# Performance work log

Hardware: AMD Instinct MI355X
Metric: run time of the kernel (lower is better)

## Reference

```python
import jax, jax.numpy as jnp
import numpy as np

L = 2        # num_layers
H = 512      # hidden_size
IN = 32      # input_size = output_size + 24
OUT = 8      # output_size
B = 512      # batch
S = 128      # encoder seq_len
F = 48       # future_len
TF = 24      # time-feature dim


def setup_inputs() -> dict:
    key = jax.random.key(0)
    ks = jax.random.split(key, 14)
    def rn(k, shape, s=0.05):
        return jax.random.normal(k, shape, dtype=jnp.float32) * s
    return {
        "x": rn(ks[0], (S, B, IN), 1.0),
        "future_time": rn(ks[1], (F - 1, B, TF), 1.0),
        "h0": rn(ks[2], (L, 1, H), 1.0),
        "c0": rn(ks[3], (L, 1, H), 1.0),
        # PyTorch nn.LSTM weights: gate order (i, f, g, o), rows of 4H
        "w_ih0": rn(ks[4], (4 * H, IN)),
        "w_hh0": rn(ks[5], (4 * H, H)),
        "b_ih0": rn(ks[6], (4 * H,)),
        "b_hh0": rn(ks[7], (4 * H,)),
        "w_ih1": rn(ks[8], (4 * H, H)),
        "w_hh1": rn(ks[9], (4 * H, H)),
        "b_ih1": rn(ks[10], (4 * H,)),
        "b_hh1": rn(ks[11], (4 * H,)),
        "fc_w": rn(ks[12], (OUT, H)),
        "fc_b": rn(ks[13], (OUT,)),
    }


def _cell(x, h, c, w_ih, w_hh, b):
    # PyTorch LSTMCell math, gate order i,f,g,o
    gates = x @ w_ih.T + h @ w_hh.T + b  # [B, 4H]
    i, f, g, o = jnp.split(gates, 4, axis=-1)
    c2 = jax.nn.sigmoid(f) * c + jax.nn.sigmoid(i) * jnp.tanh(g)
    h2 = jax.nn.sigmoid(o) * jnp.tanh(c2)
    return h2, c2


def reference(x, future_time, h0, c0,
              w_ih0, w_hh0, b_ih0, b_hh0,
              w_ih1, w_hh1, b_ih1, b_hh1,
              fc_w, fc_b):
    batch = x.shape[1]
    params = [(w_ih0, w_hh0, b_ih0 + b_hh0),
              (w_ih1, w_hh1, b_ih1 + b_hh1)]
    h_init = jnp.broadcast_to(h0, (L, batch, H))
    c_init = jnp.broadcast_to(c0, (L, batch, H))

    def multi_step(carry, x_t):
        hs, cs = carry
        new_h, new_c = [], []
        inp = x_t
        for l, (wi, wh, b) in enumerate(params):
            h2, c2 = _cell(inp, hs[l], cs[l], wi, wh, b)
            new_h.append(h2)
            new_c.append(c2)
            inp = h2
        return (jnp.stack(new_h), jnp.stack(new_c)), inp

    # encoder pass over the conditioning sequence
    (hs, cs), outs = jax.lax.scan(multi_step, (h_init, c_init), x)
    y0 = outs[-1] @ fc_w.T + fc_b  # [B, OUT], first prediction

    def dec_step(carry, t_feat):
        hs, cs, y = carry
        x_t = jnp.concatenate([y, t_feat], axis=-1)  # [B, OUT+TF] == [B, IN]
        (hs2, cs2), h_top = multi_step((hs, cs), x_t)
        y2 = h_top @ fc_w.T + fc_b
        return (hs2, cs2, y2), y2

    _, ys = jax.lax.scan(dec_step, (hs, cs, y0), future_time)
    return jnp.concatenate([y0[None], ys], axis=0)  # [future_len, B, OUT]
```

## Files before the change

kernel.cpp:

```cpp
#include <hip/hip_runtime.h>


typedef __attribute__((ext_vector_type(8))) short bf16x8;
typedef __attribute__((ext_vector_type(16))) float f32x16;

#define MFMA32(a, b, c) __builtin_amdgcn_mfma_f32_32x32x16_bf16((a), (b), (c), 0, 0, 0)
#define DEV static __device__ __forceinline__

constexpr int kSeq = 128;
constexpr int kT = 175;
constexpr int kRB = 65536;

constexpr size_t kWsHbuf = 0;
constexpr size_t kWsYacc = 2ull * 2 * 8 * kRB;
constexpr size_t kWsCnt  = kWsYacc + 2ull * 512 * 8 * 4;
constexpr size_t kWsRc   = kWsCnt + 2ull * 8 * 128;
constexpr size_t kWsEnd  = kWsRc + 2ull * 8 * 64;
constexpr size_t kWsZeroBegin = kWsYacc;
constexpr size_t kWsZeroSize  = kWsEnd - kWsYacc;

DEV unsigned short f2bf(float f) {
  unsigned u = __float_as_uint(f);
  u += 0x7fffu + ((u >> 16) & 1u);
  return (unsigned short)(u >> 16);
}
DEV float bf2f(unsigned short s) { return __uint_as_float(((unsigned)s) << 16); }
DEV float sigf(float v) { return 1.0f / (1.0f + __expf(-v)); }
DEV float tanhf_(float v) { float e = __expf(2.0f * v); return 1.0f - 2.0f / (e + 1.0f); }
DEV f32x16 zero16() {
  f32x16 z;
#pragma unroll
  for (int i = 0; i < 16; ++i) z[i] = 0.0f;
  return z;
}
DEV bf16x8 pack8(const float* p) {
  float4 a = *(const float4*)p;
  float4 b = *(const float4*)(p + 4);
  bf16x8 r;
  r[0] = (short)f2bf(a.x); r[1] = (short)f2bf(a.y);
  r[2] = (short)f2bf(a.z); r[3] = (short)f2bf(a.w);
  r[4] = (short)f2bf(b.x); r[5] = (short)f2bf(b.y);
  r[6] = (short)f2bf(b.z); r[7] = (short)f2bf(b.w);
  return r;
}

DEV unsigned ald(const unsigned* p) {
  return __hip_atomic_load(p, __ATOMIC_RELAXED, __HIP_MEMORY_SCOPE_AGENT);
}
DEV unsigned long long ald64(const unsigned long long* p) {
  return __hip_atomic_load(p, __ATOMIC_RELAXED, __HIP_MEMORY_SCOPE_AGENT);
}
DEV void ast64(unsigned long long* p, unsigned long long v) {
  __hip_atomic_store(p, v, __ATOMIC_RELAXED, __HIP_MEMORY_SCOPE_AGENT);
}
DEV float aldf(const float* p) {
  return __hip_atomic_load(p, __ATOMIC_RELAXED, __HIP_MEMORY_SCOPE_AGENT);
}
DEV void astf(float* p, float v) {
  __hip_atomic_store(p, v, __ATOMIC_RELAXED, __HIP_MEMORY_SCOPE_AGENT);
}
DEV void aadd(unsigned* p) {
  __hip_atomic_fetch_add(p, 1u, __ATOMIC_RELAXED, __HIP_MEMORY_SCOPE_AGENT);
}
DEV void relwait() {
  __atomic_signal_fence(__ATOMIC_SEQ_CST);
  __builtin_amdgcn_s_waitcnt(0);
  __atomic_signal_fence(__ATOMIC_SEQ_CST);
}
DEV bool pollc(const unsigned* c0, unsigned t0, const unsigned* c1, unsigned t1) {
  const int ln = (int)(threadIdx.x & 63);
  const unsigned* p = (ln == 1) ? c1 : c0;
  const unsigned thr = (ln == 0) ? t0 : ((ln == 1) ? t1 : 0u);
  for (int it = 0; it < (1 << 22); ++it) {
    const unsigned v = (ln < 2) ? ald(p) : 0xffffffffu;
    if (__ballot(v < thr) == 0ull) {
      __atomic_signal_fence(__ATOMIC_ACQUIRE);
      return true;
    }
    __builtin_amdgcn_s_sleep(2);
  }
  return false;
}

#define PARTS_WRITE(accv, ms_, ns_)                                           \
  { const int gate_ = (ns_)*2 + gbit;                                         \
    _Pragma("unroll") for (int rg = 0; rg < 16; ++rg) {                       \
      const int r_ = (ms_)*32 + (rg & 3) + 4 * hi5 + 8 * (rg >> 2);           \
      partsB[((kw * 4 + gate_) * 64 + r_) * 17 + l15] = f2bf((accv)[rg]);     \
    } }

__global__ __launch_bounds__(256, 2) void lstm_persist(
    const float* __restrict__ x, const float* __restrict__ ft,
    const float* __restrict__ h0in, const float* __restrict__ c0in,
    const float* __restrict__ wih0, const float* __restrict__ whh0,
    const float* __restrict__ bih0, const float* __restrict__ bhh0,
    const float* __restrict__ wih1, const float* __restrict__ whh1,
    const float* __restrict__ bih1, const float* __restrict__ bhh1,
    const float* __restrict__ fcw, const float* __restrict__ fcb,
    float* __restrict__ out, char* __restrict__ ws) {
  __shared__ __attribute__((aligned(16))) unsigned short partsB[16 * 64 * 17];
  __shared__ __attribute__((aligned(16))) unsigned short xin[64 * 40];
  __shared__ __attribute__((aligned(16))) unsigned short hloc[64 * 24];
  __shared__ float biasl[4][16];
  __shared__ float fcwl[8][16];
  __shared__ unsigned bflag;

  const int bid = blockIdx.x;
  const int layer = bid >> 8;
  const int idx = bid & 255;
  const int bc = idx & 7;
  const int hc = idx >> 3;
  const int b0 = bc * 64;
  const int u0 = hc * 16;
  const int tid = threadIdx.x;
  const int kw = tid >> 6;
  const int lane = tid & 63;
  const int l31 = lane & 31, l15 = lane & 15, hi5 = lane >> 5, gbit = (lane >> 4) & 1;

  char* hbuf = ws + kWsHbuf;
  float* yacc = (float*)(ws + kWsYacc);
  unsigned* cntbase = (unsigned*)(ws + kWsCnt);
  unsigned* rc = (unsigned*)(ws + kWsRc);

  unsigned* cs0 = cntbase + (0 * 8 + bc) * 32;
  unsigned* cs1 = cntbase + (1 * 8 + bc) * 32;
  auto region = [&](int p, int l, int b) -> char* {
    return hbuf + (size_t)(((p * 2) + l) * 8 + b) * kRB;
  };

  bool alive = true;

  bf16x8 wf[2][16];
#pragma unroll
  for (int ns = 0; ns < 2; ++ns) {
    const int gate = ns * 2 + gbit;
    const int wrow = gate * 512 + u0 + l15;
    if (layer) {
#pragma unroll
      for (int m = 0; m < 16; ++m) {
        const int jg = kw + 4 * m;
        const int k0 = jg * 16 + hi5 * 8;
        const float* p = (k0 < 512) ? (wih1 + wrow * 512 + k0)
                                    : (whh1 + wrow * 512 + (k0 - 512));
        wf[ns][m] = pack8(p);
      }
    } else {
#pragma unroll
      for (int m = 0; m < 8; ++m) {
        const int jg = kw + 4 * m;
        wf[ns][m] = pack8(whh0 + wrow * 512 + jg * 16 + hi5 * 8);
      }
      if (kw < 2) wf[ns][8] = pack8(wih0 + wrow * 32 + kw * 16 + hi5 * 8);
    }
  }

  if (tid < 64) {
    const int g = tid >> 4, h = tid & 15;
    const int row = g * 512 + u0 + h;
    biasl[g][h] = layer ? (bih1[row] + bhh1[row]) : (bih0[row] + bhh0[row]);
  }
  if (layer && tid >= 64 && tid < 192) {
    const int t2 = tid - 64;
    fcwl[t2 >> 4][t2 & 15] = fcw[(t2 >> 4) * 512 + u0 + (t2 & 15)];
  }

  const int own_h = tid & 15;
  const int own_r0 = (tid >> 4) * 4;
  float cst[4];
  {
    const float cv = c0in[layer * 512 + u0 + own_h];
    cst[0] = cst[1] = cst[2] = cst[3] = cv;
  }

  {
    char* dst = region(layer ? 0 : 1, layer, bc);
    if (tid < 128) {
      const int r = tid >> 1, half = tid & 1;
      union { unsigned short s[8]; unsigned long long u[2]; } v;
#pragma unroll
      for (int k2 = 0; k2 < 8; ++k2)
        v.s[k2] = f2bf(h0in[layer * 512 + u0 + half * 8 + k2]);
      unsigned long long* dp =
          (unsigned long long*)(dst + ((u0 >> 3) + half) * 1024 + r * 16);
      ast64(dp, v.u[0]); ast64(dp + 1, v.u[1]);
    }
    relwait();
    __syncthreads();
    if (tid == 0) aadd(layer ? cs1 : cs0);
  }

  auto xin_store = [&](int r, int c4, float4 v) {
    const int gx = c4 >> 3, half = (c4 >> 2) & 1;
    uint2 pv;
    pv.x = (unsigned)f2bf(v.x) | ((unsigned)f2bf(v.y) << 16);
    pv.y = (unsigned)f2bf(v.z) | ((unsigned)f2bf(v.w) << 16);
    *(uint2*)&xin[r * 40 + ((gx ^ (r & 3)) << 3) + half * 4] = pv;
  };

  auto cell_update = [&]() {
#pragma unroll
    for (int i = 0; i < 4; ++i) {
      const int r = own_r0 + i;
      float ig = biasl[0][own_h], fg = biasl[1][own_h];
      float gg = biasl[2][own_h], og = biasl[3][own_h];
#pragma unroll
      for (int w2 = 0; w2 < 4; ++w2) {
        ig += bf2f(partsB[((w2 * 4 + 0) * 64 + r) * 17 + own_h]);
        fg += bf2f(partsB[((w2 * 4 + 1) * 64 + r) * 17 + own_h]);
        gg += bf2f(partsB[((w2 * 4 + 2) * 64 + r) * 17 + own_h]);
        og += bf2f(partsB[((w2 * 4 + 3) * 64 + r) * 17 + own_h]);
      }
      const float cv = sigf(fg) * cst[i] + sigf(ig) * tanhf_(gg);
      cst[i] = cv;
      hloc[r * 24 + own_h] = f2bf(sigf(og) * tanhf_(cv));
    }
  };

  auto h_publish = [&](char* dst) {
    if (tid < 128) {
      const int r = tid >> 1, half = tid & 1;
      union { uint4 q; unsigned long long u[2]; } v;
      v.q = *(const uint4*)&hloc[r * 24 + half * 8];
      unsigned long long* dp =
          (unsigned long long*)(dst + ((u0 >> 3) + half) * 1024 + r * 16);
      ast64(dp, v.u[0]); ast64(dp + 1, v.u[1]);
    }
  };

  if (layer == 0) {
    for (int t = 0; t < kT; ++t) {
      const unsigned c0thr = 32u * (unsigned)(t + 1);
      if (t < kSeq) {
#pragma unroll
        for (int it = 0; it < 2; ++it) {
          const int u = tid + it * 256;
          const int r = u >> 3, c4 = (u & 7) * 4;
          xin_store(r, c4, *(const float4*)&x[(size_t)(t * 512 + b0 + r) * 32 + c4]);
        }
        if (kw == 0 && alive)
          alive = pollc(cs0, c0thr, cs1, 32u * (unsigned)t);
        __syncthreads();
      } else {
        if (kw == 0 && alive)
          alive = pollc(cs0, c0thr, cs1, 32u * (unsigned)(t + 1));
        __syncthreads();
        const int q = (t - 1) & 1;
        if (tid < 128) {
          const int r = tid >> 1, o4 = (tid & 1) * 4;
          const float* yp = &yacc[(size_t)(q * 512 + b0 + r) * 8 + o4];
          float4 v;
          v.x = aldf(yp + 0); v.y = aldf(yp + 1);
          v.z = aldf(yp + 2); v.w = aldf(yp + 3);
          const float4 bb = *(const float4*)&fcb[o4];
          v.x += bb.x; v.y += bb.y; v.z += bb.z; v.w += bb.w;
          if (hc == 0)
            *(float4*)&out[(size_t)((t - kSeq) * 512 + b0 + r) * 8 + o4] = v;
          xin_store(r, o4, v);
        }
        for (int u = tid; u < 384; u += 256) {
          const int r = u / 6, m = u - r * 6;
          xin_store(r, 8 + m * 4,
                    *(const float4*)&ft[(size_t)((t - kSeq) * 512 + b0 + r) * 24 + m * 4]);
        }
        __syncthreads();
        if (tid == 0) {
          const unsigned old = __hip_atomic_fetch_add(rc + (q * 8 + bc) * 16, 1u,
                                                      __ATOMIC_RELAXED,
                                                      __HIP_MEMORY_SCOPE_AGENT);
          bflag = (old == 31u) ? 1u : 0u;
        }
        __syncthreads();
        if (bflag) {
          for (int u = tid; u < 512; u += 256)
            astf(&yacc[(size_t)q * 512 * 8 + (size_t)b0 * 8 + u], 0.0f);
          relwait();
          __syncthreads();
          if (tid == 0)
            __hip_atomic_store(rc + (q * 8 + bc) * 16, 0u, __ATOMIC_RELAXED,
                               __HIP_MEMORY_SCOPE_AGENT);
        }
      }

      f32x16 acc00 = zero16(), acc01 = zero16(), acc10 = zero16(), acc11 = zero16();
      const char* hb0 = region((t - 1) & 1, 0, bc);
      unsigned long long abuf[2][16];
#pragma unroll
      for (int i = 0; i < 4; ++i) {
        const size_t off = (size_t)((2 * (kw + 4 * i) + hi5) * 64 + l31) * 16;
        const unsigned long long* p = (const unsigned long long*)(hb0 + off);
        abuf[0][i * 4 + 0] = ald64(p);
        abuf[0][i * 4 + 1] = ald64(p + 1);
        const unsigned long long* q2 = (const unsigned long long*)(hb0 + off + 512);
        abuf[0][i * 4 + 2] = ald64(q2);
        abuf[0][i * 4 + 3] = ald64(q2 + 1);
      }
#pragma unroll
      for (int g = 0; g < 2; ++g) {
        if (g == 0) {
#pragma unroll
          for (int i = 0; i < 4; ++i) {
            const int m = 4 + i;
            const size_t off = (size_t)((2 * (kw + 4 * m) + hi5) * 64 + l31) * 16;
            const unsigned long long* p = (const unsigned long long*)(hb0 + off);
            abuf[1][i * 4 + 0] = ald64(p);
            abuf[1][i * 4 + 1] = ald64(p + 1);
            const unsigned long long* q2 = (const unsigned long long*)(hb0 + off + 512);
            abuf[1][i * 4 + 2] = ald64(q2);
            abuf[1][i * 4 + 3] = ald64(q2 + 1);
          }
        }
#pragma unroll
        for (int i = 0; i < 4; ++i) {
          const int m = g * 4 + i;
          union { unsigned long long u[2]; bf16x8 v; } a0, a1;
          a0.u[0] = abuf[g][i * 4 + 0]; a0.u[1] = abuf[g][i * 4 + 1];
          a1.u[0] = abuf[g][i * 4 + 2]; a1.u[1] = abuf[g][i * 4 + 3];
          acc00 = MFMA32(a0.v, wf[0][m], acc00);
          acc01 = MFMA32(a0.v, wf[1][m], acc01);
          acc10 = MFMA32(a1.v, wf[0][m], acc10);
          acc11 = MFMA32(a1.v, wf[1][m], acc11);
        }
      }
      if (kw < 2) {
#pragma unroll
        for (int ms = 0; ms < 2; ++ms) {
          const int r = ms * 32 + l31;
          const int gx = kw * 2 + hi5;
          const bf16x8 a = *(const bf16x8*)&xin[r * 40 + ((gx ^ (r & 3)) << 3)];
          if (ms == 0) {
            acc00 = MFMA32(a, wf[0][8], acc00);
            acc01 = MFMA32(a, wf[1][8], acc01);
          } else {
            acc10 = MFMA32(a, wf[0][8], acc10);
            acc11 = MFMA32(a, wf[1][8], acc11);
          }
        }
      }
      PARTS_WRITE(acc00, 0, 0); PARTS_WRITE(acc01, 0, 1);
      PARTS_WRITE(acc10, 1, 0); PARTS_WRITE(acc11, 1, 1);
      __syncthreads();
      cell_update();
      __syncthreads();
      h_publish(region(t & 1, 0, bc));
      relwait();
      __syncthreads();
      if (tid == 0) aadd(cs0);
    }
    if (hc == 0) {
      if (kw == 0 && alive)
        alive = pollc(cs1, 32u * (unsigned)(kT + 1), cs1, 0u);
      __syncthreads();
      for (int u = tid; u < 512; u += 256) {
        const int r = u >> 3, o = u & 7;
        out[(size_t)(47 * 512 + b0 + r) * 8 + o] =
            aldf(&yacc[(size_t)(b0 + r) * 8 + o]) + fcb[o];
      }
    }
  } else {
    for (int t = 0; t < kT; ++t) {
      if (kw == 0 && alive)
        alive = pollc(cs0, 32u * (unsigned)(t + 2), cs1, 32u * (unsigned)(t + 1));
      __syncthreads();

      f32x16 acc00 = zero16(), acc01 = zero16(), acc10 = zero16(), acc11 = zero16();
      const char* hbA = region(t & 1, 0, bc);
      const char* hbB = region(t & 1, 1, bc);
      unsigned long long abuf[2][16];
#pragma unroll
      for (int i = 0; i < 4; ++i) {
        const char* base = hbA;
        const size_t off = (size_t)((2 * (kw + 4 * i) + hi5) * 64 + l31) * 16;
        const unsigned long long* p = (const unsigned long long*)(base + off);
        abuf[0][i * 4 + 0] = ald64(p);
        abuf[0][i * 4 + 1] = ald64(p + 1);
        const unsigned long long* q2 = (const unsigned long long*)(base + off + 512);
        abuf[0][i * 4 + 2] = ald64(q2);
        abuf[0][i * 4 + 3] = ald64(q2 + 1);
      }
#pragma unroll
      for (int g = 0; g < 4; ++g) {
        if (g < 3) {
          const int gn = g + 1;
#pragma unroll
          for (int i = 0; i < 4; ++i) {
            const int m = gn * 4 + i;
            const char* base = (m < 8) ? hbA : hbB;
            const int jl = (kw + 4 * m) & 31;
            const size_t off = (size_t)((2 * jl + hi5) * 64 + l31) * 16;
            const unsigned long long* p = (const unsigned long long*)(base + off);
            abuf[gn & 1][i * 4 + 0] = ald64(p);
            abuf[gn & 1][i * 4 + 1] = ald64(p + 1);
            const unsigned long long* q2 = (const unsigned long long*)(base + off + 512);
            abuf[gn & 1][i * 4 + 2] = ald64(q2);
            abuf[gn & 1][i * 4 + 3] = ald64(q2 + 1);
          }
        }
#pragma unroll
        for (int i = 0; i < 4; ++i) {
          const int m = g * 4 + i;
          union { unsigned long long u[2]; bf16x8 v; } a0, a1;
          a0.u[0] = abuf[g & 1][i * 4 + 0]; a0.u[1] = abuf[g & 1][i * 4 + 1];
          a1.u[0] = abuf[g & 1][i * 4 + 2]; a1.u[1] = abuf[g & 1][i * 4 + 3];
          acc00 = MFMA32(a0.v, wf[0][m], acc00);
          acc01 = MFMA32(a0.v, wf[1][m], acc01);
          acc10 = MFMA32(a1.v, wf[0][m], acc10);
          acc11 = MFMA32(a1.v, wf[1][m], acc11);
        }
      }
      PARTS_WRITE(acc00, 0, 0); PARTS_WRITE(acc01, 0, 1);
      PARTS_WRITE(acc10, 1, 0); PARTS_WRITE(acc11, 1, 1);
      __syncthreads();
      cell_update();
      __syncthreads();
      h_publish(region((t & 1) ^ 1, 1, bc));
      if (t >= kSeq - 1) {
        const int q = t & 1;
#pragma unroll
        for (int rep = 0; rep < 2; ++rep) {
          const int i2 = tid + rep * 256;
          const int r = i2 >> 3, o = i2 & 7;
          float s = 0.0f;
#pragma unroll
          for (int h2 = 0; h2 < 16; ++h2)
            s += bf2f(hloc[r * 24 + h2]) * fcwl[o][h2];
          atomicAdd(&yacc[(size_t)(q * 512 + b0 + r) * 8 + o], s);
        }
      }
      relwait();
      __syncthreads();
      if (tid == 0) aadd(cs1);
    }
  }
}

extern "C" void kernel_launch(void* const* d_in, const int* in_sizes, int n_in,
                              void* d_out, int out_size, void* d_ws, size_t ws_size,
                              hipStream_t stream) {
  (void)in_sizes; (void)n_in; (void)out_size; (void)ws_size;
  hipMemsetAsync((char*)d_ws + kWsZeroBegin, 0, kWsZeroSize, stream);

  const float* x    = (const float*)d_in[0];
  const float* ft   = (const float*)d_in[1];
  const float* h0in = (const float*)d_in[2];
  const float* c0in = (const float*)d_in[3];
  const float* wih0 = (const float*)d_in[4];
  const float* whh0 = (const float*)d_in[5];
  const float* bih0 = (const float*)d_in[6];
  const float* bhh0 = (const float*)d_in[7];
  const float* wih1 = (const float*)d_in[8];
  const float* whh1 = (const float*)d_in[9];
  const float* bih1 = (const float*)d_in[10];
  const float* bhh1 = (const float*)d_in[11];
  const float* fcw  = (const float*)d_in[12];
  const float* fcb  = (const float*)d_in[13];
  float* out = (float*)d_out;
  char* ws = (char*)d_ws;

  void* args[] = {&x, &ft, &h0in, &c0in, &wih0, &whh0, &bih0, &bhh0,
                  &wih1, &whh1, &bih1, &bhh1, &fcw, &fcb, &out, &ws};
  hipError_t err = hipLaunchCooperativeKernel((void*)lstm_persist, dim3(512),
                                              dim3(256), args, 0, stream);
  if (err != hipSuccess) {
    lstm_persist<<<dim3(512), dim3(256), 0, stream>>>(
        x, ft, h0in, c0in, wih0, whh0, bih0, bhh0,
        wih1, whh1, bih1, bhh1, fcw, fcb, out, ws);
  }
}
```

Before: 3.732 ms.

## Replace shared-counter polling with replicated generation flags; keep gate partials fp32

Blocks still increment a per-batch-chunk arrival counter. The last arriver now publishes the step generation to four replicated flag cache lines, and each block polls its own replica instead of the contended counter. This aims to reduce atomic and polling contention on one cache line in the persistent recurrence. Gate partial sums are also stored in shared memory as fp32 rather than bf16, which doubles LDS footprint and removes conversions while improving accuracy.

```diff
diff --git a/kernel.cpp b/kernel.cpp
--- a/kernel.cpp
+++ b/kernel.cpp
@@ -14,7 +14,8 @@
 constexpr size_t kWsHbuf = 0;
 constexpr size_t kWsYacc = 2ull * 2 * 8 * kRB;
 constexpr size_t kWsCnt  = kWsYacc + 2ull * 512 * 8 * 4;
-constexpr size_t kWsRc   = kWsCnt + 2ull * 8 * 128;
+constexpr size_t kWsBc   = kWsCnt + 2ull * 8 * 128;
+constexpr size_t kWsRc   = kWsBc + 2ull * 8 * 4 * 64;
 constexpr size_t kWsEnd  = kWsRc + 2ull * 8 * 64;
 constexpr size_t kWsZeroBegin = kWsYacc;
 constexpr size_t kWsZeroSize  = kWsEnd - kWsYacc;
@@ -47,6 +48,9 @@
 DEV unsigned ald(const unsigned* p) {
   return __hip_atomic_load(p, __ATOMIC_RELAXED, __HIP_MEMORY_SCOPE_AGENT);
 }
+DEV void ast(unsigned* p, unsigned v) {
+  __hip_atomic_store(p, v, __ATOMIC_RELAXED, __HIP_MEMORY_SCOPE_AGENT);
+}
 DEV unsigned long long ald64(const unsigned long long* p) {
   return __hip_atomic_load(p, __ATOMIC_RELAXED, __HIP_MEMORY_SCOPE_AGENT);
 }
@@ -59,21 +63,21 @@
 DEV void astf(float* p, float v) {
   __hip_atomic_store(p, v, __ATOMIC_RELAXED, __HIP_MEMORY_SCOPE_AGENT);
 }
-DEV void aadd(unsigned* p) {
-  __hip_atomic_fetch_add(p, 1u, __ATOMIC_RELAXED, __HIP_MEMORY_SCOPE_AGENT);
+DEV unsigned afadd(unsigned* p) {
+  return __hip_atomic_fetch_add(p, 1u, __ATOMIC_RELAXED, __HIP_MEMORY_SCOPE_AGENT);
 }
 DEV void relwait() {
   __atomic_signal_fence(__ATOMIC_SEQ_CST);
   __builtin_amdgcn_s_waitcnt(0);
   __atomic_signal_fence(__ATOMIC_SEQ_CST);
 }
-DEV bool pollc(const unsigned* c0, unsigned t0, const unsigned* c1, unsigned t1) {
+DEV bool pollb(const unsigned* p0, unsigned t0, const unsigned* p1, unsigned t1) {
   const int ln = (int)(threadIdx.x & 63);
-  const unsigned* p = (ln == 1) ? c1 : c0;
+  const unsigned* p = (ln == 1) ? p1 : p0;
   const unsigned thr = (ln == 0) ? t0 : ((ln == 1) ? t1 : 0u);
   for (int it = 0; it < (1 << 22); ++it) {
     const unsigned v = (ln < 2) ? ald(p) : 0xffffffffu;
-    if (__ballot(v < thr) == 0ull) {
+    if (__ballot((ln < 2) && (v < thr)) == 0ull) {
       __atomic_signal_fence(__ATOMIC_ACQUIRE);
       return true;
     }
@@ -86,7 +90,7 @@
   { const int gate_ = (ns_)*2 + gbit;                                         \
     _Pragma("unroll") for (int rg = 0; rg < 16; ++rg) {                       \
       const int r_ = (ms_)*32 + (rg & 3) + 4 * hi5 + 8 * (rg >> 2);           \
-      partsB[((kw * 4 + gate_) * 64 + r_) * 17 + l15] = f2bf((accv)[rg]);     \
+      partsF[((kw * 4 + gate_) * 64 + r_) * 17 + l15] = (accv)[rg];           \
     } }
 
 __global__ __launch_bounds__(256, 2) void lstm_persist(
@@ -98,7 +102,7 @@
     const float* __restrict__ bih1, const float* __restrict__ bhh1,
     const float* __restrict__ fcw, const float* __restrict__ fcb,
     float* __restrict__ out, char* __restrict__ ws) {
-  __shared__ __attribute__((aligned(16))) unsigned short partsB[16 * 64 * 17];
+  __shared__ __attribute__((aligned(16))) float partsF[16 * 64 * 17];
   __shared__ __attribute__((aligned(16))) unsigned short xin[64 * 40];
   __shared__ __attribute__((aligned(16))) unsigned short hloc[64 * 24];
   __shared__ float biasl[4][16];
@@ -119,13 +123,26 @@
 
   char* hbuf = ws + kWsHbuf;
   float* yacc = (float*)(ws + kWsYacc);
-  unsigned* cntbase = (unsigned*)(ws + kWsCnt);
+  unsigned* cntb = (unsigned*)(ws + kWsCnt);
+  unsigned* bcb = (unsigned*)(ws + kWsBc);
   unsigned* rc = (unsigned*)(ws + kWsRc);
 
-  unsigned* cs0 = cntbase + (0 * 8 + bc) * 32;
-  unsigned* cs1 = cntbase + (1 * 8 + bc) * 32;
+  unsigned* cnt0 = cntb + (0 * 8 + bc) * 32;
+  unsigned* cnt1 = cntb + (1 * 8 + bc) * 32;
+  const int rep = hc & 3;
+  unsigned* b0l = bcb + ((0 * 8 + bc) * 4 + rep) * 16;
+  unsigned* b1l = bcb + ((1 * 8 + bc) * 4 + rep) * 16;
   auto region = [&](int p, int l, int b) -> char* {
     return hbuf + (size_t)(((p * 2) + l) * 8 + b) * kRB;
+  };
+  auto signal = [&](unsigned* cl, int lyr) {
+    const unsigned old = afadd(cl);
+    if ((old & 31u) == 31u) {
+      const unsigned v = (old + 1u) >> 5;
+      unsigned* base = bcb + (lyr * 8 + bc) * 4 * 16;
+#pragma unroll
+      for (int r2 = 0; r2 < 4; ++r2) ast(base + r2 * 16, v);
+    }
   };
 
   bool alive = true;
@@ -186,7 +203,7 @@
     }
     relwait();
     __syncthreads();
-    if (tid == 0) aadd(layer ? cs1 : cs0);
+    if (tid == 0) signal(layer ? cnt1 : cnt0, layer);
   }
 
   auto xin_store = [&](int r, int c4, float4 v) {
@@ -205,10 +222,10 @@
       float gg = biasl[2][own_h], og = biasl[3][own_h];
 #pragma unroll
       for (int w2 = 0; w2 < 4; ++w2) {
-        ig += bf2f(partsB[((w2 * 4 + 0) * 64 + r) * 17 + own_h]);
-        fg += bf2f(partsB[((w2 * 4 + 1) * 64 + r) * 17 + own_h]);
-        gg += bf2f(partsB[((w2 * 4 + 2) * 64 + r) * 17 + own_h]);
-        og += bf2f(partsB[((w2 * 4 + 3) * 64 + r) * 17 + own_h]);
+        ig += partsF[((w2 * 4 + 0) * 64 + r) * 17 + own_h];
+        fg += partsF[((w2 * 4 + 1) * 64 + r) * 17 + own_h];
+        gg += partsF[((w2 * 4 + 2) * 64 + r) * 17 + own_h];
+        og += partsF[((w2 * 4 + 3) * 64 + r) * 17 + own_h];
       }
       const float cv = sigf(fg) * cst[i] + sigf(ig) * tanhf_(gg);
       cst[i] = cv;
@@ -229,7 +246,6 @@
 
   if (layer == 0) {
     for (int t = 0; t < kT; ++t) {
-      const unsigned c0thr = 32u * (unsigned)(t + 1);
       if (t < kSeq) {
 #pragma unroll
         for (int it = 0; it < 2; ++it) {
@@ -238,11 +254,11 @@
           xin_store(r, c4, *(const float4*)&x[(size_t)(t * 512 + b0 + r) * 32 + c4]);
         }
         if (kw == 0 && alive)
-          alive = pollc(cs0, c0thr, cs1, 32u * (unsigned)t);
+          alive = pollb(b0l, (unsigned)(t + 1), b1l, (unsigned)t);
         __syncthreads();
       } else {
         if (kw == 0 && alive)
-          alive = pollc(cs0, c0thr, cs1, 32u * (unsigned)(t + 1));
+          alive = pollb(b0l, (unsigned)(t + 1), b1l, (unsigned)(t + 1));
         __syncthreads();
         const int q = (t - 1) & 1;
         if (tid < 128) {
@@ -264,9 +280,7 @@
         }
         __syncthreads();
         if (tid == 0) {
-          const unsigned old = __hip_atomic_fetch_add(rc + (q * 8 + bc) * 16, 1u,
-                                                      __ATOMIC_RELAXED,
-                                                      __HIP_MEMORY_SCOPE_AGENT);
+          const unsigned old = afadd(rc + (q * 8 + bc) * 16);
           bflag = (old == 31u) ? 1u : 0u;
         }
         __syncthreads();
@@ -344,11 +358,11 @@
       h_publish(region(t & 1, 0, bc));
       relwait();
       __syncthreads();
-      if (tid == 0) aadd(cs0);
+      if (tid == 0) signal(cnt0, 0);
     }
     if (hc == 0) {
       if (kw == 0 && alive)
-        alive = pollc(cs1, 32u * (unsigned)(kT + 1), cs1, 0u);
+        alive = pollb(b1l, (unsigned)(kT + 1), b1l, (unsigned)(kT + 1));
       __syncthreads();
       for (int u = tid; u < 512; u += 256) {
         const int r = u >> 3, o = u & 7;
@@ -359,7 +373,7 @@
   } else {
     for (int t = 0; t < kT; ++t) {
       if (kw == 0 && alive)
-        alive = pollc(cs0, 32u * (unsigned)(t + 2), cs1, 32u * (unsigned)(t + 1));
+        alive = pollb(b0l, (unsigned)(t + 2), b1l, (unsigned)(t + 1));
       __syncthreads();
 
       f32x16 acc00 = zero16(), acc01 = zero16(), acc10 = zero16(), acc11 = zero16();
@@ -416,8 +430,8 @@
       if (t >= kSeq - 1) {
         const int q = t & 1;
 #pragma unroll
-        for (int rep = 0; rep < 2; ++rep) {
-          const int i2 = tid + rep * 256;
+        for (int rep2 = 0; rep2 < 2; ++rep2) {
+          const int i2 = tid + rep2 * 256;
           const int r = i2 >> 3, o = i2 & 7;
           float s = 0.0f;
 #pragma unroll
@@ -428,7 +442,7 @@
       }
       relwait();
       __syncthreads();
-      if (tid == 0) aadd(cs1);
+      if (tid == 0) signal(cnt1, 1);
     }
   }
 }
```

Measured after the change: 3.477 ms. 1.07x faster.
